# Performance work log

Hardware: AMD Instinct MI355X
Metric: run time of the kernel (lower is better)

The kernel has to match this reference:

```python
import jax, jax.numpy as jnp
import numpy as np

N_NODES = 100_000
N_EDGES = 1_600_000
NODE_FEATURES = 22


def setup_inputs() -> dict:
    key = jax.random.key(0)
    ks = jax.random.split(key, 10)
    s = 0.1
    x = jax.random.normal(ks[0], (N_NODES, NODE_FEATURES), dtype=jnp.float32)
    edge_index = jax.random.randint(ks[1], (2, N_EDGES), 0, N_NODES, dtype=jnp.int64)
    return {
        "x": x,
        "edge_index": edge_index,
        "W_embed": jax.random.normal(ks[2], (NODE_FEATURES, 32), jnp.float32) * s,
        "b_embed": jax.random.normal(ks[3], (32,), jnp.float32) * s,
        "W1": jax.random.normal(ks[4], (32, 32), jnp.float32) * s,
        "b1": jax.random.normal(ks[5], (32,), jnp.float32) * s,
        "W2": jax.random.normal(ks[6], (64, 32), jnp.float32) * s,
        "b2": jax.random.normal(ks[7], (32,), jnp.float32) * s,
        "W_pred": jax.random.normal(ks[8], (64, 1), jnp.float32) * s,
        "b_pred": jax.random.normal(ks[9], (1,), jnp.float32) * s,
    }


def gcn_conv(h, src, dst, deg_inv_sqrt, W, b, num_nodes):
    """PyG GCNConv: h' = scatter_add(norm_ij * (h W)[src] -> dst) + b.
    src/dst already include self-loops; deg_inv_sqrt precomputed on dst."""
    h = h @ W  # [N, out]
    norm = deg_inv_sqrt[src] * deg_inv_sqrt[dst]  # [E]
    msg = h[src] * norm[:, None]  # gather + normalize
    out = jax.ops.segment_sum(msg, dst, num_segments=num_nodes)  # scatter-add
    return out + b


def reference(x, edge_index, W_embed, b_embed, W1, b1, W2, b2, W_pred, b_pred):
    n = x.shape[0]
    loop = jnp.arange(n, dtype=edge_index.dtype)
    src = jnp.concatenate([edge_index[0], loop])  # add self-loops
    dst = jnp.concatenate([edge_index[1], loop])
    deg = jax.ops.segment_sum(jnp.ones_like(src, dtype=x.dtype), dst, num_segments=n)
    deg_inv_sqrt = jnp.where(deg > 0, jax.lax.rsqrt(jnp.maximum(deg, 1.0)), 0.0)

    h = x @ W_embed + b_embed  # MLP_embed
    # dropout is identity at eval time
    h0 = h
    h = gcn_conv(h, src, dst, deg_inv_sqrt, W1, b1, n)
    h = jax.nn.relu(h)
    h = jnp.concatenate([h, h0], axis=1)  # [N, 64]
    h = gcn_conv(h, src, dst, deg_inv_sqrt, W2, b2, n)
    h = jax.nn.relu(h)
    h = jnp.concatenate([h, h0], axis=1)  # [N, 64]
    delta = h @ W_pred + b_pred  # [N, 1]
    out = jax.nn.relu(delta + x[:, 1:2])
    return out
```

## Files before the change

kernel.cpp:

```cpp
#include <hip/hip_runtime.h>
#include <hip/hip_bf16.h>

#define NF 22
#define H  32
#define BSH 8
#define CAP 8192
#define CHUNK 2048

__device__ __forceinline__ float bflo(unsigned int v) { return __uint_as_float(v << 16); }
__device__ __forceinline__ float bfhi(unsigned int v) { return __uint_as_float(v & 0xffff0000u); }
__device__ __forceinline__ unsigned int packbf2(float a, float b) {
    __hip_bfloat162 p; p.x = __float2bfloat16(a); p.y = __float2bfloat16(b);
    return *(unsigned int*)&p;
}

__global__ void init_cur(int* __restrict__ cursor, int NB) {
    int i = blockIdx.x * blockDim.x + threadIdx.x;
    if (i < NB) cursor[i] = i * CAP;
}

__global__ __launch_bounds__(256) void bin_edges(
    const int* __restrict__ src, const int* __restrict__ dst,
    int* __restrict__ cursor, int* __restrict__ binned, int E, int NB)
{
    __shared__ int lh[512];
    __shared__ int lcur[512];
    int tid = threadIdx.x;
    for (int j = tid; j < NB; j += 256) lh[j] = 0;
    __syncthreads();
    int e0 = blockIdx.x * CHUNK;
    int ee = min(e0 + CHUNK, E);
    for (int i = e0 + tid; i < ee; i += 256) atomicAdd(&lh[dst[i] >> BSH], 1);
    __syncthreads();
    for (int j = tid; j < NB; j += 256) {
        int c = lh[j];
        if (c) lcur[j] = atomicAdd(&cursor[j], c);
    }
    __syncthreads();
    for (int i = e0 + tid; i < ee; i += 256) {
        int d = dst[i];
        int p = atomicAdd(&lcur[d >> BSH], 1);
        binned[p] = (src[i] << BSH) | (d & 255);
    }
}

__global__ __launch_bounds__(1024) void bucket_csr(
    const int* __restrict__ cursor, const int* __restrict__ binned,
    int* __restrict__ rowptr, int* __restrict__ rowcnt, int* __restrict__ sorted_src,
    float* __restrict__ dis, int N)
{
    __shared__ int cnt[256];
    __shared__ int s[256];
    __shared__ int lcur[256];
    int b = blockIdx.x, tid = threadIdx.x;
    int bn = b << BSH;
    if (tid < 256) cnt[tid] = 0;
    __syncthreads();
    int es = b * CAP, ee = cursor[b];
    for (int i = es + tid; i < ee; i += 1024) atomicAdd(&cnt[binned[i] & 255], 1);
    __syncthreads();
    int v = 0;
    if (tid < 256) { v = cnt[tid]; s[tid] = v; }
    __syncthreads();
    for (int off = 1; off < 256; off <<= 1) {
        int t = 0;
        if (tid < 256 && tid >= off) t = s[tid - off];
        __syncthreads();
        if (tid < 256) s[tid] += t;
        __syncthreads();
    }
    if (tid < 256) {
        int ex = s[tid] - v;
        lcur[tid] = ex;
        int n = bn + tid;
        if (n < N) {
            rowptr[n] = es + ex;
            rowcnt[n] = v;
            dis[n] = rsqrtf((float)(v + 1));
        }
    }
    __syncthreads();
    for (int i = es + tid; i < ee; i += 1024) {
        int e = binned[i];
        int p = atomicAdd(&lcur[e & 255], 1);
        sorted_src[es + p] = e >> BSH;
    }
}

__global__ __launch_bounds__(256) void embed_g1(
    const float* __restrict__ x, const float* __restrict__ We,
    const float* __restrict__ be, const float* __restrict__ W1,
    const float* __restrict__ W2, const float* __restrict__ Wp,
    const float* __restrict__ bp, const float* __restrict__ dis,
    __hip_bfloat16* __restrict__ g, __hip_bfloat16* __restrict__ y2,
    float* __restrict__ hp, int N)
{
    __shared__ float sWe[NF * H];
    __shared__ float sW1[H * H];
    __shared__ float sW2b[H * H];
    __shared__ float sbe[H];
    __shared__ float sWpb[H];
    __shared__ float sx[8][NF];
    __shared__ float sh[8][H];

    int tid = threadIdx.x;
    for (int j = tid; j < NF * H; j += 256) sWe[j] = We[j];
    for (int j = tid; j < H * H; j += 256) sW1[j] = W1[j];
    for (int j = tid; j < H * H; j += 256) sW2b[j] = W2[H * H + j];
    if (tid < H) sbe[tid] = be[tid];
    if (tid >= H && tid < 2 * H) sWpb[tid - H] = Wp[tid];

    int grp = tid >> 5, t = tid & 31;
    int ngrp = (N + 7) >> 3;
    for (int nb = blockIdx.x; nb < ngrp; nb += gridDim.x) {
        int node = nb * 8 + grp;
        int nodec = node < N ? node : N - 1;
        __syncthreads();
        if (t < NF) sx[grp][t] = x[(size_t)nodec * NF + t];
        __syncthreads();

        float h = sbe[t];
#pragma unroll
        for (int k = 0; k < NF; k++) h += sx[grp][k] * sWe[k * H + t];
        sh[grp][t] = h;
        __syncthreads();

        float di = dis[nodec];
        float gv = 0.f, yv = 0.f;
#pragma unroll
        for (int k = 0; k < H; k++) {
            float hv = sh[grp][k];
            gv += hv * sW1[k * H + t];
            yv += hv * sW2b[k * H + t];
        }
        gv *= di;

        float pv = h * sWpb[t];
#pragma unroll
        for (int off = 16; off > 0; off >>= 1) pv += __shfl_down(pv, off, 32);

        if (node < N) {
            size_t o = (size_t)node * H + t;
            g[o] = __float2bfloat16(gv);
            y2[o] = __float2bfloat16(yv);
            if (t == 0) hp[node] = pv + bp[0] + sx[grp][1];
        }
    }
}

__global__ __launch_bounds__(256) void agg_mid(
    const int* __restrict__ rowptr, const int* __restrict__ rowcnt,
    const int* __restrict__ sorted_src,
    const __hip_bfloat16* __restrict__ g_in, const __hip_bfloat16* __restrict__ y2,
    const float* __restrict__ dis, const float* __restrict__ W2,
    const float* __restrict__ b1, __hip_bfloat16* __restrict__ g_out, int N)
{
    __shared__ float sW2[H * H];
    __shared__ float srow[32][33];

    int tid = threadIdx.x;
    for (int j = tid; j < H * H; j += 256) sW2[j] = W2[j];

    int grp = tid >> 3, lane = tid & 7;
    int node = blockIdx.x * 32 + grp;
    int nodec = node < N ? node : N - 1;

    const uint2* gv2 = (const uint2*)g_in;
    uint2 sv = gv2[(size_t)nodec * 8 + lane];
    float a0 = bflo(sv.x), a1 = bfhi(sv.x), a2 = bflo(sv.y), a3 = bfhi(sv.y);

    int start = rowptr[nodec];
    int end = start + rowcnt[nodec];
    int i = start;
    for (; i + 7 < end; i += 8) {
        int s0 = sorted_src[i],     s1 = sorted_src[i + 1];
        int s2 = sorted_src[i + 2], s3 = sorted_src[i + 3];
        int s4 = sorted_src[i + 4], s5 = sorted_src[i + 5];
        int s6 = sorted_src[i + 6], s7 = sorted_src[i + 7];
        uint2 v0 = gv2[(size_t)s0 * 8 + lane], v1 = gv2[(size_t)s1 * 8 + lane];
        uint2 v2 = gv2[(size_t)s2 * 8 + lane], v3 = gv2[(size_t)s3 * 8 + lane];
        uint2 v4 = gv2[(size_t)s4 * 8 + lane], v5 = gv2[(size_t)s5 * 8 + lane];
        uint2 v6 = gv2[(size_t)s6 * 8 + lane], v7 = gv2[(size_t)s7 * 8 + lane];
        a0 += bflo(v0.x) + bflo(v1.x) + bflo(v2.x) + bflo(v3.x)
            + bflo(v4.x) + bflo(v5.x) + bflo(v6.x) + bflo(v7.x);
        a1 += bfhi(v0.x) + bfhi(v1.x) + bfhi(v2.x) + bfhi(v3.x)
            + bfhi(v4.x) + bfhi(v5.x) + bfhi(v6.x) + bfhi(v7.x);
        a2 += bflo(v0.y) + bflo(v1.y) + bflo(v2.y) + bflo(v3.y)
            + bflo(v4.y) + bflo(v5.y) + bflo(v6.y) + bflo(v7.y);
        a3 += bfhi(v0.y) + bfhi(v1.y) + bfhi(v2.y) + bfhi(v3.y)
            + bfhi(v4.y) + bfhi(v5.y) + bfhi(v6.y) + bfhi(v7.y);
    }
    for (; i < end; i++) {
        uint2 v = gv2[(size_t)sorted_src[i] * 8 + lane];
        a0 += bflo(v.x); a1 += bfhi(v.x); a2 += bflo(v.y); a3 += bfhi(v.y);
    }

    float di = dis[nodec];
    float4 bb = ((const float4*)b1)[lane];
    srow[grp][4 * lane]     = fmaxf(di * a0 + bb.x, 0.f);
    srow[grp][4 * lane + 1] = fmaxf(di * a1 + bb.y, 0.f);
    srow[grp][4 * lane + 2] = fmaxf(di * a2 + bb.z, 0.f);
    srow[grp][4 * lane + 3] = fmaxf(di * a3 + bb.w, 0.f);
    __syncthreads();

    const float4* sW2v = (const float4*)sW2;
    float o0 = 0.f, o1 = 0.f, o2 = 0.f, o3 = 0.f;
#pragma unroll
    for (int k = 0; k < H; k++) {
        float rv = srow[grp][k];
        float4 w = sW2v[k * 8 + lane];
        o0 += rv * w.x; o1 += rv * w.y; o2 += rv * w.z; o3 += rv * w.w;
    }
    uint2 yv = ((const uint2*)y2)[(size_t)nodec * 8 + lane];
    o0 = di * (o0 + bflo(yv.x));
    o1 = di * (o1 + bfhi(yv.x));
    o2 = di * (o2 + bflo(yv.y));
    o3 = di * (o3 + bfhi(yv.y));

    if (node < N) {
        uint2 p;
        p.x = packbf2(o0, o1);
        p.y = packbf2(o2, o3);
        ((uint2*)g_out)[(size_t)node * 8 + lane] = p;
    }
}

__global__ __launch_bounds__(256) void agg_final(
    const int* __restrict__ rowptr, const int* __restrict__ rowcnt,
    const int* __restrict__ sorted_src,
    const __hip_bfloat16* __restrict__ g_in, const float* __restrict__ hp,
    const float* __restrict__ dis, const float* __restrict__ b2,
    const float* __restrict__ Wp, float* __restrict__ out, int N)
{
    int gid = blockIdx.x * blockDim.x + threadIdx.x;
    int node = gid >> 3;
    if (node >= N) return;
    int lane = gid & 7;

    const uint2* gv2 = (const uint2*)g_in;
    uint2 sv = gv2[(size_t)node * 8 + lane];
    float a0 = bflo(sv.x), a1 = bfhi(sv.x), a2 = bflo(sv.y), a3 = bfhi(sv.y);

    int start = rowptr[node];
    int end = start + rowcnt[node];
    int i = start;
    for (; i + 7 < end; i += 8) {
        int s0 = sorted_src[i],     s1 = sorted_src[i + 1];
        int s2 = sorted_src[i + 2], s3 = sorted_src[i + 3];
        int s4 = sorted_src[i + 4], s5 = sorted_src[i + 5];
        int s6 = sorted_src[i + 6], s7 = sorted_src[i + 7];
        uint2 v0 = gv2[(size_t)s0 * 8 + lane], v1 = gv2[(size_t)s1 * 8 + lane];
        uint2 v2 = gv2[(size_t)s2 * 8 + lane], v3 = gv2[(size_t)s3 * 8 + lane];
        uint2 v4 = gv2[(size_t)s4 * 8 + lane], v5 = gv2[(size_t)s5 * 8 + lane];
        uint2 v6 = gv2[(size_t)s6 * 8 + lane], v7 = gv2[(size_t)s7 * 8 + lane];
        a0 += bflo(v0.x) + bflo(v1.x) + bflo(v2.x) + bflo(v3.x)
            + bflo(v4.x) + bflo(v5.x) + bflo(v6.x) + bflo(v7.x);
        a1 += bfhi(v0.x) + bfhi(v1.x) + bfhi(v2.x) + bfhi(v3.x)
            + bfhi(v4.x) + bfhi(v5.x) + bfhi(v6.x) + bfhi(v7.x);
        a2 += bflo(v0.y) + bflo(v1.y) + bflo(v2.y) + bflo(v3.y)
            + bflo(v4.y) + bflo(v5.y) + bflo(v6.y) + bflo(v7.y);
        a3 += bfhi(v0.y) + bfhi(v1.y) + bfhi(v2.y) + bfhi(v3.y)
            + bfhi(v4.y) + bfhi(v5.y) + bfhi(v6.y) + bfhi(v7.y);
    }
    for (; i < end; i++) {
        uint2 v = gv2[(size_t)sorted_src[i] * 8 + lane];
        a0 += bflo(v.x); a1 += bfhi(v.x); a2 += bflo(v.y); a3 += bfhi(v.y);
    }

    float di = dis[node];
    float4 b2v = ((const float4*)b2)[lane];
    float4 wp  = ((const float4*)Wp)[lane];
    float v = fmaxf(di * a0 + b2v.x, 0.f) * wp.x
            + fmaxf(di * a1 + b2v.y, 0.f) * wp.y
            + fmaxf(di * a2 + b2v.z, 0.f) * wp.z
            + fmaxf(di * a3 + b2v.w, 0.f) * wp.w;
#pragma unroll
    for (int off = 4; off > 0; off >>= 1) v += __shfl_down(v, off, 8);
    if (lane == 0) out[node] = fmaxf(v + hp[node], 0.f);
}

extern "C" void kernel_launch(void* const* d_in, const int* in_sizes, int n_in,
                              void* d_out, int out_size, void* d_ws, size_t ws_size,
                              hipStream_t stream) {
    const float* x  = (const float*)d_in[0];
    const int*   ei = (const int*)d_in[1];
    const float* We = (const float*)d_in[2];
    const float* be = (const float*)d_in[3];
    const float* W1 = (const float*)d_in[4];
    const float* b1 = (const float*)d_in[5];
    const float* W2 = (const float*)d_in[6];
    const float* b2 = (const float*)d_in[7];
    const float* Wp = (const float*)d_in[8];
    const float* bp = (const float*)d_in[9];
    float* out = (float*)d_out;

    const int N = in_sizes[0] / NF;
    const int E = in_sizes[1] / 2;
    const int* src = ei;
    const int* dst = ei + E;
    const int NB = (N + 255) >> BSH;
    const int nchunk = (E + CHUNK - 1) / CHUNK;

    size_t Np  = ((size_t)N + 127) & ~(size_t)127;
    size_t NHp = ((size_t)N * H + 127) & ~(size_t)127;
    float* ws  = (float*)d_ws;
    float* dis = ws;
    float* hp  = dis + Np;
    __hip_bfloat16* g1 = (__hip_bfloat16*)(hp + Np);
    __hip_bfloat16* g2 = g1 + NHp;
    __hip_bfloat16* y2 = g2 + NHp;
    int* cursor     = (int*)(y2 + NHp);
    int* rowptr     = cursor + 512;
    int* rowcnt     = rowptr + Np;
    int* binned     = rowcnt + Np;
    int* sorted_src = binned + (size_t)NB * CAP;

    init_cur<<<2, 256, 0, stream>>>(cursor, NB);
    bin_edges<<<nchunk, 256, 0, stream>>>(src, dst, cursor, binned, E, NB);
    bucket_csr<<<NB, 1024, 0, stream>>>(cursor, binned, rowptr, rowcnt, sorted_src, dis, N);

    int ngrp = (N + 7) >> 3;
    int eg = ngrp < 1536 ? ngrp : 1536;
    embed_g1<<<eg, 256, 0, stream>>>(x, We, be, W1, W2, Wp, bp, dis, g1, y2, hp, N);
    agg_mid<<<(N + 31) / 32, 256, 0, stream>>>(rowptr, rowcnt, sorted_src, g1, y2, dis, W2, b1, g2, N);
    agg_final<<<((size_t)N * 8 + 255) / 256, 256, 0, stream>>>(rowptr, rowcnt, sorted_src, g2, hp, dis, b2, Wp, out, N);
}
```

Baseline: 217.6 us.

## Stage edge binning in shared memory for coalesced bucket writes

```diff
diff --git a/kernel.cpp b/kernel.cpp
--- a/kernel.cpp
+++ b/kernel.cpp
@@ -5,7 +5,7 @@
 #define H  32
 #define BSH 8
 #define CAP 8192
-#define CHUNK 2048
+#define BCHUNK 4096
 
 __device__ __forceinline__ float bflo(unsigned int v) { return __uint_as_float(v << 16); }
 __device__ __forceinline__ float bfhi(unsigned int v) { return __uint_as_float(v & 0xffff0000u); }
@@ -19,28 +19,63 @@
     if (i < NB) cursor[i] = i * CAP;
 }
 
-__global__ __launch_bounds__(256) void bin_edges(
+__global__ __launch_bounds__(512) void bin_edges(
     const int* __restrict__ src, const int* __restrict__ dst,
     int* __restrict__ cursor, int* __restrict__ binned, int E, int NB)
 {
-    __shared__ int lh[512];
+    __shared__ int vals[BCHUNK];
+    __shared__ unsigned short bkts[BCHUNK];
+    __shared__ int svals[BCHUNK];
+    __shared__ unsigned short sbkt[BCHUNK];
+    __shared__ int scnt[512];
+    __shared__ int sex[512];
     __shared__ int lcur[512];
+    __shared__ int gbase[512];
+
     int tid = threadIdx.x;
-    for (int j = tid; j < NB; j += 256) lh[j] = 0;
-    __syncthreads();
-    int e0 = blockIdx.x * CHUNK;
-    int ee = min(e0 + CHUNK, E);
-    for (int i = e0 + tid; i < ee; i += 256) atomicAdd(&lh[dst[i] >> BSH], 1);
-    __syncthreads();
-    for (int j = tid; j < NB; j += 256) {
-        int c = lh[j];
-        if (c) lcur[j] = atomicAdd(&cursor[j], c);
-    }
-    __syncthreads();
-    for (int i = e0 + tid; i < ee; i += 256) {
-        int d = dst[i];
-        int p = atomicAdd(&lcur[d >> BSH], 1);
-        binned[p] = (src[i] << BSH) | (d & 255);
+    for (int j = tid; j < NB; j += 512) scnt[j] = 0;
+    __syncthreads();
+
+    int e0 = blockIdx.x * BCHUNK;
+    int n = min(e0 + BCHUNK, E) - e0;
+
+    for (int i = tid; i < n; i += 512) {
+        int d = dst[e0 + i];
+        int b = d >> BSH;
+        vals[i] = (src[e0 + i] << BSH) | (d & 255);
+        bkts[i] = (unsigned short)b;
+        atomicAdd(&scnt[b], 1);
+    }
+    __syncthreads();
+
+    int c = (tid < NB) ? scnt[tid] : 0;
+    int acc = c;
+    sex[tid] = acc;
+    __syncthreads();
+    for (int off = 1; off < 512; off <<= 1) {
+        int t = (tid >= off) ? sex[tid - off] : 0;
+        __syncthreads();
+        sex[tid] += t;
+        __syncthreads();
+    }
+    int ex = sex[tid] - acc;
+    __syncthreads();
+    sex[tid] = ex;
+    lcur[tid] = ex;
+    if (tid < NB && c) gbase[tid] = atomicAdd(&cursor[tid], c);
+    __syncthreads();
+
+    for (int i = tid; i < n; i += 512) {
+        int b = bkts[i];
+        int p = atomicAdd(&lcur[b], 1);
+        svals[p] = vals[i];
+        sbkt[p] = (unsigned short)b;
+    }
+    __syncthreads();
+
+    for (int i = tid; i < n; i += 512) {
+        int b = sbkt[i];
+        binned[gbase[b] + (i - sex[b])] = svals[i];
     }
 }
 
@@ -299,7 +334,7 @@
     const int* src = ei;
     const int* dst = ei + E;
     const int NB = (N + 255) >> BSH;
-    const int nchunk = (E + CHUNK - 1) / CHUNK;
+    const int nchunk = (E + BCHUNK - 1) / BCHUNK;
 
     size_t Np  = ((size_t)N + 127) & ~(size_t)127;
     size_t NHp = ((size_t)N * H + 127) & ~(size_t)127;
@@ -316,7 +351,7 @@
     int* sorted_src = binned + (size_t)NB * CAP;
 
     init_cur<<<2, 256, 0, stream>>>(cursor, NB);
-    bin_edges<<<nchunk, 256, 0, stream>>>(src, dst, cursor, binned, E, NB);
+    bin_edges<<<nchunk, 512, 0, stream>>>(src, dst, cursor, binned, E, NB);
     bucket_csr<<<NB, 1024, 0, stream>>>(cursor, binned, rowptr, rowcnt, sorted_src, dis, N);
 
     int ngrp = (N + 7) >> 3;
```

Result: faster. 196.3 us (-9.8%).
